# Kernel optimization log

Hardware: AMD Instinct MI355X
Metric: run time of the kernel (lower is better)

Reference implementation:

```python
import jax, jax.numpy as jnp
import numpy as np

N, E, D, G = 20000, 640000, 256, 64
BN_EPS = 1e-5


def setup_inputs() -> dict:
    key = jax.random.key(0)
    ks = jax.random.split(key, 16)
    p = lambda k, sh: jax.random.normal(k, sh, dtype=jnp.float32) * 0.05
    x = jax.random.normal(ks[0], (N, D), dtype=jnp.float32)
    edge_index = jax.random.randint(ks[1], (2, E), 0, N, dtype=jnp.int32)
    batch = jnp.sort(jax.random.randint(ks[2], (N,), 0, G, dtype=jnp.int32))
    return dict(
        x=x, edge_index=edge_index, batch=batch,
        W1=p(ks[3], (D, D)), a1_src=p(ks[4], (D,)), a1_dst=p(ks[5], (D,)), b1=p(ks[6], (D,)),
        W2=p(ks[7], (D, D)), a2_src=p(ks[8], (D,)), a2_dst=p(ks[9], (D,)), b2=p(ks[10], (D,)),
        bn_gamma=jnp.ones((D,), jnp.float32), bn_beta=jnp.zeros((D,), jnp.float32),
        bn_mean=jnp.zeros((D,), jnp.float32), bn_var=jnp.ones((D,), jnp.float32),
        Wl=p(ks[11], (D, D)), bl=p(ks[12], (D,)),
    )


def gat_conv(x, src, dst, W, a_src, a_dst, b):
    # PyG GATConv, heads=1, concat=True, negative_slope=0.2, self-loops already appended
    h = x @ W                               # [N, D]
    alpha_s = h @ a_src                     # [N]
    alpha_d = h @ a_dst                     # [N]
    e = jax.nn.leaky_relu(alpha_s[src] + alpha_d[dst], 0.2)   # [E+N]
    # segment softmax over edges grouped by destination node
    m = jax.ops.segment_max(e, dst, num_segments=N)
    ex = jnp.exp(e - m[dst])
    s = jax.ops.segment_sum(ex, dst, num_segments=N)
    alpha = ex / s[dst]                     # self-loops guarantee s > 0
    out = jax.ops.segment_sum(alpha[:, None] * h[src], dst, num_segments=N)
    return out + b


def reference(x, edge_index, batch, W1, a1_src, a1_dst, b1, W2, a2_src, a2_dst, b2,
              bn_gamma, bn_beta, bn_mean, bn_var, Wl, bl):
    loop = jnp.arange(N, dtype=edge_index.dtype)
    src = jnp.concatenate([edge_index[0], loop])
    dst = jnp.concatenate([edge_index[1], loop])

    h = jax.nn.leaky_relu(gat_conv(x, src, dst, W1, a1_src, a1_dst, b1), 0.01)
    h = jax.nn.leaky_relu(gat_conv(h, src, dst, W2, a2_src, a2_dst, b2), 0.01)
    # BatchNorm over nodes (eval mode, running stats)
    h = (h - bn_mean) * jax.lax.rsqrt(bn_var + BN_EPS) * bn_gamma + bn_beta
    # global mean pool per graph, then linear (dropout is identity in eval)
    sums = jax.ops.segment_sum(h, batch, num_segments=G)           # [G, D]
    cnt = jax.ops.segment_sum(jnp.ones((N,), h.dtype), batch, num_segments=G)
    pooled = sums / jnp.maximum(cnt, 1.0)[:, None]
    return pooled @ Wl.T + bl
```

## Files before the change

### kernel.cpp

```cpp
#include <hip/hip_runtime.h>
#include <hip/hip_bf16.h>

#define NN 20000
#define EE 640000
#define DD 256
#define GG 64
#define ETOT (EE + NN)
#define BN_EPS 1e-5f

#define NPART 8
#define PBLK  128
#define CE    (EE / PBLK)
#define PRNG  (NN / NPART)

#define GBM 64
#define GBN 128
#define GBK 64
#define NGEMMB 626

typedef short s16x8 __attribute__((ext_vector_type(8)));
typedef float f32x4 __attribute__((ext_vector_type(4)));
typedef int   i32x2 __attribute__((ext_vector_type(2)));

__device__ __forceinline__ unsigned short f2bf_hi(float x) {
    unsigned u = __float_as_uint(x);
    unsigned r = (u + 0x7FFFu + ((u >> 16) & 1u)) >> 16;
    return (unsigned short)r;
}
__device__ __forceinline__ float bf2f(unsigned short h) {
    return __uint_as_float(((unsigned)h) << 16);
}

__device__ __forceinline__ void gemm_body(short* As_h, short* As_l,
                                          short* Bs_h, short* Bs_l,
                                          int gx, int gy,
                                          const float* __restrict__ A,
                                          const short* __restrict__ BhT,
                                          const short* __restrict__ BlT,
                                          const float* __restrict__ a_src,
                                          const float* __restrict__ a_dst,
                                          short* __restrict__ hb,
                                          float* __restrict__ asp,
                                          float* __restrict__ adp, int M) {
    int tid = threadIdx.x;
    int row0 = gy * GBM;
    int col0 = gx * GBN;
    int w = tid >> 6, lane = tid & 63;
    int wr = w >> 1, wc = w & 1;

    f32x4 acc[2][4];
    #pragma unroll
    for (int m = 0; m < 2; ++m)
        #pragma unroll
        for (int n = 0; n < 4; ++n)
            acc[m][n] = (f32x4){0.f, 0.f, 0.f, 0.f};

    int srow = tid >> 3;
    int sslot = tid & 7;

    for (int k0 = 0; k0 < DD; k0 += GBK) {
        __syncthreads();
        #pragma unroll
        for (int p = 0; p < 2; ++p) {
            int r = p * 32 + srow;
            int gr = row0 + r;
            float xv[8];
            if (gr < M) {
                const float4* ap = (const float4*)(A + (size_t)gr * DD + k0 + sslot * 8);
                float4 a0 = ap[0], a1 = ap[1];
                xv[0] = a0.x; xv[1] = a0.y; xv[2] = a0.z; xv[3] = a0.w;
                xv[4] = a1.x; xv[5] = a1.y; xv[6] = a1.z; xv[7] = a1.w;
            } else {
                #pragma unroll
                for (int i = 0; i < 8; ++i) xv[i] = 0.f;
            }
            s16x8 hv, lv;
            #pragma unroll
            for (int i = 0; i < 8; ++i) {
                unsigned short hbb = f2bf_hi(xv[i]);
                hv[i] = (short)hbb;
                lv[i] = (short)f2bf_hi(xv[i] - bf2f(hbb));
            }
            int byte = r * 128 + ((sslot ^ (r & 7)) << 4);
            *(s16x8*)((char*)As_h + byte) = hv;
            *(s16x8*)((char*)As_l + byte) = lv;
        }
        #pragma unroll
        for (int p = 0; p < 4; ++p) {
            int r = p * 32 + srow;
            int byte = r * 128 + ((sslot ^ (r & 7)) << 4);
            const short* bhp = BhT + (size_t)(col0 + r) * DD + k0 + sslot * 8;
            const short* blp = BlT + (size_t)(col0 + r) * DD + k0 + sslot * 8;
            *(s16x8*)((char*)Bs_h + byte) = *(const s16x8*)bhp;
            *(s16x8*)((char*)Bs_l + byte) = *(const s16x8*)blp;
        }
        __syncthreads();

        #pragma unroll
        for (int ks = 0; ks < 2; ++ks) {
            s16x8 ah[2], al[2], bh[4], bl[4];
            int g = ks * 4 + (lane >> 4);
            #pragma unroll
            for (int m = 0; m < 2; ++m) {
                int r = wr * 32 + m * 16 + (lane & 15);
                int byte = r * 128 + ((g ^ (r & 7)) << 4);
                ah[m] = *(const s16x8*)((char*)As_h + byte);
                al[m] = *(const s16x8*)((char*)As_l + byte);
            }
            #pragma unroll
            for (int n = 0; n < 4; ++n) {
                int c = wc * 64 + n * 16 + (lane & 15);
                int byte = c * 128 + ((g ^ (c & 7)) << 4);
                bh[n] = *(const s16x8*)((char*)Bs_h + byte);
                bl[n] = *(const s16x8*)((char*)Bs_l + byte);
            }
            #pragma unroll
            for (int m = 0; m < 2; ++m)
                #pragma unroll
                for (int n = 0; n < 4; ++n) {
                    acc[m][n] = __builtin_amdgcn_mfma_f32_16x16x32_bf16(ah[m], bh[n], acc[m][n], 0, 0, 0);
                    acc[m][n] = __builtin_amdgcn_mfma_f32_16x16x32_bf16(ah[m], bl[n], acc[m][n], 0, 0, 0);
                    acc[m][n] = __builtin_amdgcn_mfma_f32_16x16x32_bf16(al[m], bh[n], acc[m][n], 0, 0, 0);
                }
        }
    }

    float vsrc[4], vdst[4];
    #pragma unroll
    for (int n = 0; n < 4; ++n) {
        int cg = col0 + wc * 64 + n * 16 + (lane & 15);
        vsrc[n] = a_src[cg];
        vdst[n] = a_dst[cg];
    }
    #pragma unroll
    for (int m = 0; m < 2; ++m) {
        #pragma unroll
        for (int j = 0; j < 4; ++j) {
            float ps = 0.f, pd = 0.f;
            #pragma unroll
            for (int n = 0; n < 4; ++n) {
                float c = acc[m][n][j];
                ps += c * vsrc[n];
                pd += c * vdst[n];
            }
            #pragma unroll
            for (int o = 1; o < 16; o <<= 1) {
                ps += __shfl_xor(ps, o, 64);
                pd += __shfl_xor(pd, o, 64);
            }
            if ((lane & 15) == 0) {
                int rg = row0 + wr * 32 + m * 16 + ((lane >> 4) << 2) + j;
                if (rg < M) {
                    asp[(size_t)(gx * 2 + wc) * NN + rg] = ps;
                    adp[(size_t)(gx * 2 + wc) * NN + rg] = pd;
                }
            }
        }
    }

    #pragma unroll
    for (int m = 0; m < 2; ++m) {
        int rbase = row0 + wr * 32 + m * 16 + ((lane >> 4) << 2);
        #pragma unroll
        for (int n = 0; n < 4; ++n) {
            int cg = col0 + wc * 64 + n * 16 + (lane & 15);
            #pragma unroll
            for (int j = 0; j < 4; ++j) {
                int rg = rbase + j;
                if (rg < M) hb[(size_t)rg * DD + cg] = (short)f2bf_hi(acc[m][n][j]);
            }
        }
    }
}

__global__ __launch_bounds__(256) void prep_hist_conv_kernel(
        const int* __restrict__ batch, int* __restrict__ start, float* __restrict__ cntf,
        const int* __restrict__ ei, int* __restrict__ counts,
        const float* __restrict__ W1, const float* __restrict__ W2,
        short* __restrict__ BhT1, short* __restrict__ BlT1,
        short* __restrict__ BhT2, short* __restrict__ BlT2) {
    int b = blockIdx.x;
    int r = b & 15, G = b >> 4;
    if (r < 8) {
        int lo = (b & 7) * PRNG;
        int e0 = G * CE;
        for (int i = e0 + threadIdx.x; i < e0 + CE; i += 256) {
            int d = ei[EE + i];
            if ((unsigned)(d - lo) < (unsigned)PRNG) atomicAdd(&counts[d], 1);
        }
        return;
    }
    int idx = G * 8 + (r - 8);
    if (idx < 512) {
        int n = idx & 255, which = idx >> 8;
        int k = threadIdx.x;
        const float* B = which ? W2 : W1;
        short* Bh = which ? BhT2 : BhT1;
        short* Bl = which ? BlT2 : BlT1;
        float x = B[k * DD + n];
        unsigned short hbv = f2bf_hi(x);
        Bh[n * DD + k] = (short)hbv;
        Bl[n * DD + k] = (short)f2bf_hi(x - bf2f(hbv));
    } else if (idx == 512) {
        int g = threadIdx.x;
        if (g <= GG) {
            if (g == GG) start[GG] = NN;
            else {
                int lo = 0, hi = NN;
                while (lo < hi) { int mid = (lo + hi) >> 1; if (batch[mid] < g) lo = mid + 1; else hi = mid; }
                start[g] = lo;
            }
        }
        __syncthreads();
        if (g < GG) cntf[g] = (float)(start[g + 1] - start[g]);
    }
}

#define SCHUNK 20
__global__ __launch_bounds__(1024) void scan_kernel(const int* __restrict__ counts,
                                                    int* __restrict__ offsets,
                                                    int* __restrict__ cursor) {
    __shared__ int wsums[16];
    int t = threadIdx.x, lane = t & 63, wid = t >> 6;
    int base = t * SCHUNK;
    int loc[SCHUNK];
    int sum = 0;
    #pragma unroll
    for (int i = 0; i < SCHUNK; ++i) {
        int idx = base + i;
        int v = (idx < NN) ? (counts[idx] + 1) : 0;
        loc[i] = sum; sum += v;
    }
    int x = sum;
    #pragma unroll
    for (int o = 1; o < 64; o <<= 1) { int tv = __shfl_up(x, o, 64); if (lane >= o) x += tv; }
    if (lane == 63) wsums[wid] = x;
    __syncthreads();
    if (wid == 0) {
        int wv = (lane < 16) ? wsums[lane] : 0;
        #pragma unroll
        for (int o = 1; o < 16; o <<= 1) { int tv = __shfl_up(wv, o, 64); if (lane >= o) wv += tv; }
        if (lane < 16) wsums[lane] = wv;
    }
    __syncthreads();
    int tbase = (wid ? wsums[wid - 1] : 0) + x - sum;
    #pragma unroll
    for (int i = 0; i < SCHUNK; ++i) {
        int idx = base + i;
        if (idx < NN) { int e = tbase + loc[i]; offsets[idx] = e; cursor[idx] = e; }
    }
    if (t == 0) offsets[NN] = wsums[15];
}

__global__ __launch_bounds__(256) void gemm_scatter_kernel(
        const int* __restrict__ ei, int* __restrict__ cursor, int* __restrict__ csr_src,
        const float* __restrict__ A,
        const short* __restrict__ BhT, const short* __restrict__ BlT,
        const float* __restrict__ a_src, const float* __restrict__ a_dst,
        short* __restrict__ hb, float* __restrict__ asp, float* __restrict__ adp, int M) {
    __shared__ short As_h[GBM * GBK];
    __shared__ short As_l[GBM * GBK];
    __shared__ short Bs_h[GBN * GBK];
    __shared__ short Bs_l[GBN * GBK];
    int b = blockIdx.x;
    int r = b & 15, G = b >> 4;
    if (r < 8) {
        int lo = (b & 7) * PRNG;
        int e0 = G * CE;
        for (int i = e0 + threadIdx.x; i < e0 + CE; i += 256) {
            int d = ei[EE + i];
            if ((unsigned)(d - lo) < (unsigned)PRNG) {
                int pos = atomicAdd(&cursor[d], 1);
                csr_src[pos] = ei[i];
            }
        }
        return;
    }
    int gidx = G * 8 + (r - 8);
    if (gidx >= NGEMMB) return;
    gemm_body(As_h, As_l, Bs_h, Bs_l, gidx & 1, gidx >> 1,
              A, BhT, BlT, a_src, a_dst, hb, asp, adp, M);
}

__global__ __launch_bounds__(256) void gemm_kernel(
        const float* __restrict__ A,
        const short* __restrict__ BhT, const short* __restrict__ BlT,
        const float* __restrict__ a_src, const float* __restrict__ a_dst,
        short* __restrict__ hb, float* __restrict__ asp, float* __restrict__ adp, int M) {
    __shared__ short As_h[GBM * GBK];
    __shared__ short As_l[GBM * GBK];
    __shared__ short Bs_h[GBN * GBK];
    __shared__ short Bs_l[GBN * GBK];
    int gidx = blockIdx.x;
    gemm_body(As_h, As_l, Bs_h, Bs_l, gidx & 1, gidx >> 1,
              A, BhT, BlT, a_src, a_dst, hb, asp, adp, M);
}

__global__ void reduce_kernel(const float* __restrict__ asp, const float* __restrict__ adp,
                              const int* __restrict__ offsets,
                              float* __restrict__ as_, float* __restrict__ ad_,
                              int* __restrict__ csr_src) {
    int i = blockIdx.x * blockDim.x + threadIdx.x;
    if (i < NN) {
        as_[i] = asp[i] + asp[NN + i] + asp[2 * NN + i] + asp[3 * NN + i];
        ad_[i] = adp[i] + adp[NN + i] + adp[2 * NN + i] + adp[3 * NN + i];
        csr_src[offsets[i + 1] - 1] = i;
    }
}

__global__ __launch_bounds__(256) void alpha_kernel(const int* __restrict__ csr_src,
                                                    const int* __restrict__ offsets,
                                                    const float* __restrict__ as_,
                                                    const float* __restrict__ ad_,
                                                    int2* __restrict__ pairs) {
    int tid = threadIdx.x;
    int w = tid >> 6, lane = tid & 63;
    int node = blockIdx.x * 4 + w;
    int off = offsets[node];
    int deg = offsets[node + 1] - off;
    float adn = ad_[node];

    if (deg <= 64) {
        int si = 0; float e = -INFINITY;
        if (lane < deg) {
            si = csr_src[off + lane];
            float t = as_[si] + adn;
            e = (t > 0.f) ? t : 0.2f * t;
        }
        float m = e;
        #pragma unroll
        for (int o = 32; o > 0; o >>= 1) m = fmaxf(m, __shfl_xor(m, o, 64));
        float ex = (lane < deg) ? expf(e - m) : 0.f;
        float s = ex;
        #pragma unroll
        for (int o = 32; o > 0; o >>= 1) s += __shfl_xor(s, o, 64);
        if (lane < deg) {
            int2 p; p.x = si; p.y = __float_as_int(ex / s);
            pairs[off + lane] = p;
        }
        return;
    }

    float m = -INFINITY, s = 0.f;
    for (int cs = 0; cs < deg; cs += 64) {
        int cl = min(64, deg - cs);
        float e = -INFINITY;
        if (lane < cl) {
            int si = csr_src[off + cs + lane];
            float t = as_[si] + adn;
            e = (t > 0.f) ? t : 0.2f * t;
        }
        float cm = e;
        #pragma unroll
        for (int o = 32; o > 0; o >>= 1) cm = fmaxf(cm, __shfl_xor(cm, o, 64));
        float newm = fmaxf(m, cm);
        float ex = (lane < cl) ? expf(e - newm) : 0.f;
        float csum = ex;
        #pragma unroll
        for (int o = 32; o > 0; o >>= 1) csum += __shfl_xor(csum, o, 64);
        s = s * expf(m - newm) + csum;
        m = newm;
    }
    float inv = 1.f / s;
    for (int cs = 0; cs < deg; cs += 64) {
        int cl = min(64, deg - cs);
        if (lane < cl) {
            int si = csr_src[off + cs + lane];
            float t = as_[si] + adn;
            float e = (t > 0.f) ? t : 0.2f * t;
            int2 p; p.x = si; p.y = __float_as_int(expf(e - m) * inv);
            pairs[off + cs + lane] = p;
        }
    }
}

__global__ __launch_bounds__(256) void aggregate_kernel(const short* __restrict__ hb,
                                                        const int2* __restrict__ pairs,
                                                        const int* __restrict__ offsets,
                                                        const float* __restrict__ bias,
                                                        float* __restrict__ out) {
    int tid = threadIdx.x;
    int w = tid >> 6, lane = tid & 63;
    int b = blockIdx.x;
    int sl = b & 3;
    int node = ((b >> 2) << 2) + w;
    int eg = lane >> 3;
    int fl = lane & 7;
    int f0 = sl * 64 + fl * 8;
    int off = offsets[node];
    int deg = offsets[node + 1] - off;
    const i32x2* pp = (const i32x2*)pairs + off;

    float acc[4][8];
    #pragma unroll
    for (int c = 0; c < 4; ++c)
        #pragma unroll
        for (int k = 0; k < 8; ++k) acc[c][k] = 0.f;

    for (int j0 = 0; j0 < deg; j0 += 32) {
        i32x2 q[4];
        float a[4];
        #pragma unroll
        for (int c = 0; c < 4; ++c) {
            int idx = j0 + c * 8 + eg;
            int idxc = (idx < deg) ? idx : 0;
            q[c] = pp[idxc];
            a[c] = (idx < deg) ? __int_as_float(q[c].y) : 0.f;
        }
        #pragma unroll
        for (int c = 0; c < 4; ++c) {
            s16x8 hv = *(const s16x8*)(hb + (size_t)q[c].x * DD + f0);
            #pragma unroll
            for (int k = 0; k < 8; ++k)
                acc[c][k] += a[c] * bf2f((unsigned short)hv[k]);
        }
    }

    f32x4 r0, r1;
    #pragma unroll
    for (int k = 0; k < 8; ++k) {
        float v = (acc[0][k] + acc[1][k]) + (acc[2][k] + acc[3][k]);
        v += __shfl_xor(v, 8, 64);
        v += __shfl_xor(v, 16, 64);
        v += __shfl_xor(v, 32, 64);
        if (k < 4) r0[k] = v; else r1[k - 4] = v;
    }
    if (eg == 0) {
        const f32x4 b0 = *(const f32x4*)(bias + f0);
        const f32x4 b1 = *(const f32x4*)(bias + f0 + 4);
        #pragma unroll
        for (int k = 0; k < 4; ++k) {
            float v0 = r0[k] + b0[k];
            float v1 = r1[k] + b1[k];
            r0[k] = (v0 > 0.f) ? v0 : 0.01f * v0;
            r1[k] = (v1 > 0.f) ? v1 : 0.01f * v1;
        }
        __builtin_nontemporal_store(r0, (f32x4*)(out + (size_t)node * DD + f0));
        __builtin_nontemporal_store(r1, (f32x4*)(out + (size_t)node * DD + f0 + 4));
    }
}

#define PSLICE 8
__global__ __launch_bounds__(256) void pool_kernel(const float* __restrict__ h,
                                                   const int* __restrict__ start,
                                                   float* __restrict__ pool) {
    int g = blockIdx.x >> 3, sl = blockIdx.x & (PSLICE - 1);
    int f = threadIdx.x;
    int s0 = start[g], s1 = start[g + 1];
    float acc = 0.f;
    for (int nd = s0 + sl; nd < s1; nd += PSLICE)
        acc += h[(size_t)nd * DD + f];
    if (acc != 0.f || sl == 0) atomicAdd(&pool[g * DD + f], acc);
}

__global__ __launch_bounds__(256) void final_kernel(const float* __restrict__ pool,
                                                    const float* __restrict__ cnt,
                                                    const float* __restrict__ gam,
                                                    const float* __restrict__ bet,
                                                    const float* __restrict__ mean,
                                                    const float* __restrict__ var,
                                                    const float* __restrict__ Wl,
                                                    const float* __restrict__ bl,
                                                    float* __restrict__ out) {
    __shared__ float p_sh[DD];
    int g = blockIdx.x, j = threadIdx.x;
    float cn = cnt[g];
    float scale = gam[j] * rsqrtf(var[j] + BN_EPS);
    p_sh[j] = (cn > 0.f) ? (pool[g * DD + j] / cn - mean[j]) * scale + bet[j] : 0.f;
    __syncthreads();
    float acc = 0.f;
    for (int fi = 0; fi < DD; ++fi)
        acc += p_sh[fi] * Wl[j * DD + fi];
    out[g * DD + j] = acc + bl[j];
}

extern "C" void kernel_launch(void* const* d_in, const int* in_sizes, int n_in,
                              void* d_out, int out_size, void* d_ws, size_t ws_size,
                              hipStream_t stream) {
    const float* x       = (const float*)d_in[0];
    const int*   ei      = (const int*)d_in[1];
    const int*   batch   = (const int*)d_in[2];
    const float* W1      = (const float*)d_in[3];
    const float* a1_src  = (const float*)d_in[4];
    const float* a1_dst  = (const float*)d_in[5];
    const float* b1      = (const float*)d_in[6];
    const float* W2      = (const float*)d_in[7];
    const float* a2_src  = (const float*)d_in[8];
    const float* a2_dst  = (const float*)d_in[9];
    const float* b2      = (const float*)d_in[10];
    const float* bn_g    = (const float*)d_in[11];
    const float* bn_b    = (const float*)d_in[12];
    const float* bn_m    = (const float*)d_in[13];
    const float* bn_v    = (const float*)d_in[14];
    const float* Wl      = (const float*)d_in[15];
    const float* bl      = (const float*)d_in[16];
    float* out = (float*)d_out;

    char* ws = (char*)d_ws;
    size_t o = 0;
    auto take = [&](size_t bytes) { char* p = ws + o; o += (bytes + 255) & ~(size_t)255; return p; };
    int*   counts  = (int*)  take(NN * 4);
    int*   offsets = (int*)  take((NN + 1) * 4);
    int*   cursor  = (int*)  take(NN * 4);
    int*   csr_src = (int*)  take((size_t)ETOT * 4);
    int2*  pairs   = (int2*) take((size_t)ETOT * 8);
    float* asp     = (float*)take((size_t)4 * NN * 4);
    float* adp     = (float*)take((size_t)4 * NN * 4);
    float* as_     = (float*)take(NN * 4);
    float* ad_     = (float*)take(NN * 4);
    short* hb      = (short*)take((size_t)NN * DD * 2);
    float* bufB    = (float*)take((size_t)NN * DD * 4);
    float* pool    = (float*)take(GG * DD * 4);
    float* cnt     = (float*)take(GG * 4);
    int*   start   = (int*)  take((GG + 1) * 4);
    short* BhT1    = (short*)take((size_t)DD * DD * 2);
    short* BlT1    = (short*)take((size_t)DD * DD * 2);
    short* BhT2    = (short*)take((size_t)DD * DD * 2);
    short* BlT2    = (short*)take((size_t)DD * DD * 2);
    (void)ws_size; (void)in_sizes; (void)n_in; (void)out_size;

    hipMemsetAsync(counts, 0, NN * 4, stream);
    hipMemsetAsync(pool, 0, GG * DD * 4, stream);

    prep_hist_conv_kernel<<<2048, 256, 0, stream>>>(batch, start, cnt, ei, counts,
                                                    W1, W2, BhT1, BlT1, BhT2, BlT2);
    scan_kernel<<<1, 1024, 0, stream>>>(counts, offsets, cursor);

    gemm_scatter_kernel<<<2048, 256, 0, stream>>>(ei, cursor, csr_src,
                                                  x, BhT1, BlT1, a1_src, a1_dst,
                                                  hb, asp, adp, NN);
    reduce_kernel<<<(NN + 255) / 256, 256, 0, stream>>>(asp, adp, offsets, as_, ad_, csr_src);
    alpha_kernel<<<NN / 4, 256, 0, stream>>>(csr_src, offsets, as_, ad_, pairs);
    aggregate_kernel<<<NN, 256, 0, stream>>>(hb, pairs, offsets, b1, bufB);

    gemm_kernel<<<NGEMMB, 256, 0, stream>>>(bufB, BhT2, BlT2, a2_src, a2_dst, hb, asp, adp, NN);
    reduce_kernel<<<(NN + 255) / 256, 256, 0, stream>>>(asp, adp, offsets, as_, ad_, csr_src);
    alpha_kernel<<<NN / 4, 256, 0, stream>>>(csr_src, offsets, as_, ad_, pairs);
    aggregate_kernel<<<NN, 256, 0, stream>>>(hb, pairs, offsets, b2, bufB);

    pool_kernel<<<GG * PSLICE, 256, 0, stream>>>(bufB, start, pool);
    final_kernel<<<GG, 256, 0, stream>>>(pool, cnt, bn_g, bn_b, bn_m, bn_v, Wl, bl, out);
}
```

Before: 315.5 us.

## Fuse CSR scatter tail into GEMM blocks and software-pipeline aggregate gather

Layer 1's GEMM no longer interleaves with dedicated scatter blocks that each scan edges for a destination partition. Every GEMM block now does its tile and then scatters a contiguous slice of about 1023 edges into the CSR with atomics, so the partition filtering and repeated edge reads go away. The aggregate kernel now uses two accumulators and prefetches the next pair indices one step ahead, with a lighter bf16 unpack. The trade-offs are less memory-level parallelism per step in the gather and atomics to arbitrary destinations across the whole node range.

```diff
diff --git a/kernel.cpp b/kernel.cpp
--- a/kernel.cpp
+++ b/kernel.cpp
@@ -17,10 +17,12 @@
 #define GBN 128
 #define GBK 64
 #define NGEMMB 626
+#define SCE 1023
 
 typedef short s16x8 __attribute__((ext_vector_type(8)));
 typedef float f32x4 __attribute__((ext_vector_type(4)));
 typedef int   i32x2 __attribute__((ext_vector_type(2)));
+typedef int   i32x4 __attribute__((ext_vector_type(4)));
 
 __device__ __forceinline__ unsigned short f2bf_hi(float x) {
     unsigned u = __float_as_uint(x);
@@ -31,145 +33,14 @@
     return __uint_as_float(((unsigned)h) << 16);
 }
 
-__device__ __forceinline__ void gemm_body(short* As_h, short* As_l,
-                                          short* Bs_h, short* Bs_l,
-                                          int gx, int gy,
-                                          const float* __restrict__ A,
-                                          const short* __restrict__ BhT,
-                                          const short* __restrict__ BlT,
-                                          const float* __restrict__ a_src,
-                                          const float* __restrict__ a_dst,
-                                          short* __restrict__ hb,
-                                          float* __restrict__ asp,
-                                          float* __restrict__ adp, int M) {
-    int tid = threadIdx.x;
-    int row0 = gy * GBM;
-    int col0 = gx * GBN;
-    int w = tid >> 6, lane = tid & 63;
-    int wr = w >> 1, wc = w & 1;
-
-    f32x4 acc[2][4];
-    #pragma unroll
-    for (int m = 0; m < 2; ++m)
-        #pragma unroll
-        for (int n = 0; n < 4; ++n)
-            acc[m][n] = (f32x4){0.f, 0.f, 0.f, 0.f};
-
-    int srow = tid >> 3;
-    int sslot = tid & 7;
-
-    for (int k0 = 0; k0 < DD; k0 += GBK) {
-        __syncthreads();
-        #pragma unroll
-        for (int p = 0; p < 2; ++p) {
-            int r = p * 32 + srow;
-            int gr = row0 + r;
-            float xv[8];
-            if (gr < M) {
-                const float4* ap = (const float4*)(A + (size_t)gr * DD + k0 + sslot * 8);
-                float4 a0 = ap[0], a1 = ap[1];
-                xv[0] = a0.x; xv[1] = a0.y; xv[2] = a0.z; xv[3] = a0.w;
-                xv[4] = a1.x; xv[5] = a1.y; xv[6] = a1.z; xv[7] = a1.w;
-            } else {
-                #pragma unroll
-                for (int i = 0; i < 8; ++i) xv[i] = 0.f;
-            }
-            s16x8 hv, lv;
-            #pragma unroll
-            for (int i = 0; i < 8; ++i) {
-                unsigned short hbb = f2bf_hi(xv[i]);
-                hv[i] = (short)hbb;
-                lv[i] = (short)f2bf_hi(xv[i] - bf2f(hbb));
-            }
-            int byte = r * 128 + ((sslot ^ (r & 7)) << 4);
-            *(s16x8*)((char*)As_h + byte) = hv;
-            *(s16x8*)((char*)As_l + byte) = lv;
-        }
-        #pragma unroll
-        for (int p = 0; p < 4; ++p) {
-            int r = p * 32 + srow;
-            int byte = r * 128 + ((sslot ^ (r & 7)) << 4);
-            const short* bhp = BhT + (size_t)(col0 + r) * DD + k0 + sslot * 8;
-            const short* blp = BlT + (size_t)(col0 + r) * DD + k0 + sslot * 8;
-            *(s16x8*)((char*)Bs_h + byte) = *(const s16x8*)bhp;
-            *(s16x8*)((char*)Bs_l + byte) = *(const s16x8*)blp;
-        }
-        __syncthreads();
-
-        #pragma unroll
-        for (int ks = 0; ks < 2; ++ks) {
-            s16x8 ah[2], al[2], bh[4], bl[4];
-            int g = ks * 4 + (lane >> 4);
-            #pragma unroll
-            for (int m = 0; m < 2; ++m) {
-                int r = wr * 32 + m * 16 + (lane & 15);
-                int byte = r * 128 + ((g ^ (r & 7)) << 4);
-                ah[m] = *(const s16x8*)((char*)As_h + byte);
-                al[m] = *(const s16x8*)((char*)As_l + byte);
-            }
-            #pragma unroll
-            for (int n = 0; n < 4; ++n) {
-                int c = wc * 64 + n * 16 + (lane & 15);
-                int byte = c * 128 + ((g ^ (c & 7)) << 4);
-                bh[n] = *(const s16x8*)((char*)Bs_h + byte);
-                bl[n] = *(const s16x8*)((char*)Bs_l + byte);
-            }
-            #pragma unroll
-            for (int m = 0; m < 2; ++m)
-                #pragma unroll
-                for (int n = 0; n < 4; ++n) {
-                    acc[m][n] = __builtin_amdgcn_mfma_f32_16x16x32_bf16(ah[m], bh[n], acc[m][n], 0, 0, 0);
-                    acc[m][n] = __builtin_amdgcn_mfma_f32_16x16x32_bf16(ah[m], bl[n], acc[m][n], 0, 0, 0);
-                    acc[m][n] = __builtin_amdgcn_mfma_f32_16x16x32_bf16(al[m], bh[n], acc[m][n], 0, 0, 0);
-                }
-        }
-    }
-
-    float vsrc[4], vdst[4];
-    #pragma unroll
-    for (int n = 0; n < 4; ++n) {
-        int cg = col0 + wc * 64 + n * 16 + (lane & 15);
-        vsrc[n] = a_src[cg];
-        vdst[n] = a_dst[cg];
-    }
-    #pragma unroll
-    for (int m = 0; m < 2; ++m) {
-        #pragma unroll
-        for (int j = 0; j < 4; ++j) {
-            float ps = 0.f, pd = 0.f;
-            #pragma unroll
-            for (int n = 0; n < 4; ++n) {
-                float c = acc[m][n][j];
-                ps += c * vsrc[n];
-                pd += c * vdst[n];
-            }
-            #pragma unroll
-            for (int o = 1; o < 16; o <<= 1) {
-                ps += __shfl_xor(ps, o, 64);
-                pd += __shfl_xor(pd, o, 64);
-            }
-            if ((lane & 15) == 0) {
-                int rg = row0 + wr * 32 + m * 16 + ((lane >> 4) << 2) + j;
-                if (rg < M) {
-                    asp[(size_t)(gx * 2 + wc) * NN + rg] = ps;
-                    adp[(size_t)(gx * 2 + wc) * NN + rg] = pd;
-                }
-            }
-        }
-    }
-
-    #pragma unroll
-    for (int m = 0; m < 2; ++m) {
-        int rbase = row0 + wr * 32 + m * 16 + ((lane >> 4) << 2);
-        #pragma unroll
-        for (int n = 0; n < 4; ++n) {
-            int cg = col0 + wc * 64 + n * 16 + (lane & 15);
-            #pragma unroll
-            for (int j = 0; j < 4; ++j) {
-                int rg = rbase + j;
-                if (rg < M) hb[(size_t)rg * DD + cg] = (short)f2bf_hi(acc[m][n][j]);
-            }
-        }
+__device__ __forceinline__ void fma8(const short* __restrict__ hb, int row, int f0,
+                                     float a, float* acc) {
+    i32x4 hv = *(const i32x4*)(hb + (size_t)row * DD + f0);
+    #pragma unroll
+    for (int k = 0; k < 4; ++k) {
+        unsigned u = (unsigned)hv[k];
+        acc[2 * k]     += a * __uint_as_float(u << 16);
+        acc[2 * k + 1] += a * __uint_as_float(u & 0xFFFF0000u);
     }
 }
 
@@ -252,48 +123,158 @@
     if (t == 0) offsets[NN] = wsums[15];
 }
 
-__global__ __launch_bounds__(256) void gemm_scatter_kernel(
-        const int* __restrict__ ei, int* __restrict__ cursor, int* __restrict__ csr_src,
+template<bool SCAT>
+__global__ __launch_bounds__(256) void gemm_kernel(
         const float* __restrict__ A,
         const short* __restrict__ BhT, const short* __restrict__ BlT,
         const float* __restrict__ a_src, const float* __restrict__ a_dst,
-        short* __restrict__ hb, float* __restrict__ asp, float* __restrict__ adp, int M) {
+        short* __restrict__ hb, float* __restrict__ asp, float* __restrict__ adp, int M,
+        const int* __restrict__ ei, int* __restrict__ cursor, int* __restrict__ csr_src) {
     __shared__ short As_h[GBM * GBK];
     __shared__ short As_l[GBM * GBK];
     __shared__ short Bs_h[GBN * GBK];
     __shared__ short Bs_l[GBN * GBK];
-    int b = blockIdx.x;
-    int r = b & 15, G = b >> 4;
-    if (r < 8) {
-        int lo = (b & 7) * PRNG;
-        int e0 = G * CE;
-        for (int i = e0 + threadIdx.x; i < e0 + CE; i += 256) {
+    int tid = threadIdx.x;
+    int gx = blockIdx.x, gy = blockIdx.y;
+    int row0 = gy * GBM;
+    int col0 = gx * GBN;
+    int w = tid >> 6, lane = tid & 63;
+    int wr = w >> 1, wc = w & 1;
+
+    f32x4 acc[2][4];
+    #pragma unroll
+    for (int m = 0; m < 2; ++m)
+        #pragma unroll
+        for (int n = 0; n < 4; ++n)
+            acc[m][n] = (f32x4){0.f, 0.f, 0.f, 0.f};
+
+    int srow = tid >> 3;
+    int sslot = tid & 7;
+
+    for (int k0 = 0; k0 < DD; k0 += GBK) {
+        __syncthreads();
+        #pragma unroll
+        for (int p = 0; p < 2; ++p) {
+            int r = p * 32 + srow;
+            int gr = row0 + r;
+            float xv[8];
+            if (gr < M) {
+                const float4* ap = (const float4*)(A + (size_t)gr * DD + k0 + sslot * 8);
+                float4 a0 = ap[0], a1 = ap[1];
+                xv[0] = a0.x; xv[1] = a0.y; xv[2] = a0.z; xv[3] = a0.w;
+                xv[4] = a1.x; xv[5] = a1.y; xv[6] = a1.z; xv[7] = a1.w;
+            } else {
+                #pragma unroll
+                for (int i = 0; i < 8; ++i) xv[i] = 0.f;
+            }
+            s16x8 hv, lv;
+            #pragma unroll
+            for (int i = 0; i < 8; ++i) {
+                unsigned short hbb = f2bf_hi(xv[i]);
+                hv[i] = (short)hbb;
+                lv[i] = (short)f2bf_hi(xv[i] - bf2f(hbb));
+            }
+            int byte = r * 128 + ((sslot ^ (r & 7)) << 4);
+            *(s16x8*)((char*)As_h + byte) = hv;
+            *(s16x8*)((char*)As_l + byte) = lv;
+        }
+        #pragma unroll
+        for (int p = 0; p < 4; ++p) {
+            int r = p * 32 + srow;
+            int byte = r * 128 + ((sslot ^ (r & 7)) << 4);
+            const short* bhp = BhT + (size_t)(col0 + r) * DD + k0 + sslot * 8;
+            const short* blp = BlT + (size_t)(col0 + r) * DD + k0 + sslot * 8;
+            *(s16x8*)((char*)Bs_h + byte) = *(const s16x8*)bhp;
+            *(s16x8*)((char*)Bs_l + byte) = *(const s16x8*)blp;
+        }
+        __syncthreads();
+
+        #pragma unroll
+        for (int ks = 0; ks < 2; ++ks) {
+            s16x8 ah[2], al[2], bh[4], bl[4];
+            int g = ks * 4 + (lane >> 4);
+            #pragma unroll
+            for (int m = 0; m < 2; ++m) {
+                int r = wr * 32 + m * 16 + (lane & 15);
+                int byte = r * 128 + ((g ^ (r & 7)) << 4);
+                ah[m] = *(const s16x8*)((char*)As_h + byte);
+                al[m] = *(const s16x8*)((char*)As_l + byte);
+            }
+            #pragma unroll
+            for (int n = 0; n < 4; ++n) {
+                int c = wc * 64 + n * 16 + (lane & 15);
+                int byte = c * 128 + ((g ^ (c & 7)) << 4);
+                bh[n] = *(const s16x8*)((char*)Bs_h + byte);
+                bl[n] = *(const s16x8*)((char*)Bs_l + byte);
+            }
+            #pragma unroll
+            for (int m = 0; m < 2; ++m)
+                #pragma unroll
+                for (int n = 0; n < 4; ++n) {
+                    acc[m][n] = __builtin_amdgcn_mfma_f32_16x16x32_bf16(ah[m], bh[n], acc[m][n], 0, 0, 0);
+                    acc[m][n] = __builtin_amdgcn_mfma_f32_16x16x32_bf16(ah[m], bl[n], acc[m][n], 0, 0, 0);
+                    acc[m][n] = __builtin_amdgcn_mfma_f32_16x16x32_bf16(al[m], bh[n], acc[m][n], 0, 0, 0);
+                }
+        }
+    }
+
+    float vsrc[4], vdst[4];
+    #pragma unroll
+    for (int n = 0; n < 4; ++n) {
+        int cg = col0 + wc * 64 + n * 16 + (lane & 15);
+        vsrc[n] = a_src[cg];
+        vdst[n] = a_dst[cg];
+    }
+    #pragma unroll
+    for (int m = 0; m < 2; ++m) {
+        #pragma unroll
+        for (int j = 0; j < 4; ++j) {
+            float ps = 0.f, pd = 0.f;
+            #pragma unroll
+            for (int n = 0; n < 4; ++n) {
+                float c = acc[m][n][j];
+                ps += c * vsrc[n];
+                pd += c * vdst[n];
+            }
+            #pragma unroll
+            for (int o = 1; o < 16; o <<= 1) {
+                ps += __shfl_xor(ps, o, 64);
+                pd += __shfl_xor(pd, o, 64);
+            }
+            if ((lane & 15) == 0) {
+                int rg = row0 + wr * 32 + m * 16 + ((lane >> 4) << 2) + j;
+                if (rg < M) {
+                    asp[(size_t)(gx * 2 + wc) * NN + rg] = ps;
+                    adp[(size_t)(gx * 2 + wc) * NN + rg] = pd;
+                }
+            }
+        }
+    }
+
+    #pragma unroll
+    for (int m = 0; m < 2; ++m) {
+        int rbase = row0 + wr * 32 + m * 16 + ((lane >> 4) << 2);
+        #pragma unroll
+        for (int n = 0; n < 4; ++n) {
+            int cg = col0 + wc * 64 + n * 16 + (lane & 15);
+            #pragma unroll
+            for (int j = 0; j < 4; ++j) {
+                int rg = rbase + j;
+                if (rg < M) hb[(size_t)rg * DD + cg] = (short)f2bf_hi(acc[m][n][j]);
+            }
+        }
+    }
+
+    if (SCAT) {
+        int bid = gy * 2 + gx;
+        int e0 = bid * SCE;
+        int e1 = min(e0 + SCE, EE);
+        for (int i = e0 + tid; i < e1; i += 256) {
             int d = ei[EE + i];
-            if ((unsigned)(d - lo) < (unsigned)PRNG) {
-                int pos = atomicAdd(&cursor[d], 1);
-                csr_src[pos] = ei[i];
-            }
-        }
-        return;
-    }
-    int gidx = G * 8 + (r - 8);
-    if (gidx >= NGEMMB) return;
-    gemm_body(As_h, As_l, Bs_h, Bs_l, gidx & 1, gidx >> 1,
-              A, BhT, BlT, a_src, a_dst, hb, asp, adp, M);
-}
-
-__global__ __launch_bounds__(256) void gemm_kernel(
-        const float* __restrict__ A,
-        const short* __restrict__ BhT, const short* __restrict__ BlT,
-        const float* __restrict__ a_src, const float* __restrict__ a_dst,
-        short* __restrict__ hb, float* __restrict__ asp, float* __restrict__ adp, int M) {
-    __shared__ short As_h[GBM * GBK];
-    __shared__ short As_l[GBM * GBK];
-    __shared__ short Bs_h[GBN * GBK];
-    __shared__ short Bs_l[GBN * GBK];
-    int gidx = blockIdx.x;
-    gemm_body(As_h, As_l, Bs_h, Bs_l, gidx & 1, gidx >> 1,
-              A, BhT, BlT, a_src, a_dst, hb, asp, adp, M);
+            int pos = atomicAdd(&cursor[d], 1);
+            csr_src[pos] = ei[i];
+        }
+    }
 }
 
 __global__ void reduce_kernel(const float* __restrict__ asp, const float* __restrict__ adp,
@@ -391,35 +372,40 @@
     int deg = offsets[node + 1] - off;
     const i32x2* pp = (const i32x2*)pairs + off;
 
-    float acc[4][8];
-    #pragma unroll
-    for (int c = 0; c < 4; ++c)
-        #pragma unroll
-        for (int k = 0; k < 8; ++k) acc[c][k] = 0.f;
-
-    for (int j0 = 0; j0 < deg; j0 += 32) {
-        i32x2 q[4];
-        float a[4];
-        #pragma unroll
-        for (int c = 0; c < 4; ++c) {
-            int idx = j0 + c * 8 + eg;
-            int idxc = (idx < deg) ? idx : 0;
-            q[c] = pp[idxc];
-            a[c] = (idx < deg) ? __int_as_float(q[c].y) : 0.f;
-        }
-        #pragma unroll
-        for (int c = 0; c < 4; ++c) {
-            s16x8 hv = *(const s16x8*)(hb + (size_t)q[c].x * DD + f0);
-            #pragma unroll
-            for (int k = 0; k < 8; ++k)
-                acc[c][k] += a[c] * bf2f((unsigned short)hv[k]);
+    float accA[8], accB[8];
+    #pragma unroll
+    for (int k = 0; k < 8; ++k) { accA[k] = 0.f; accB[k] = 0.f; }
+
+    int j = 0;
+    i32x2 qA, qB;
+    if (deg >= 16) { qA = pp[eg]; qB = pp[8 + eg]; }
+    for (; j + 32 <= deg; j += 16) {
+        i32x2 nA = pp[j + 16 + eg];
+        i32x2 nB = pp[j + 24 + eg];
+        fma8(hb, qA.x, f0, __int_as_float(qA.y), accA);
+        fma8(hb, qB.x, f0, __int_as_float(qB.y), accB);
+        qA = nA; qB = nB;
+    }
+    if (j + 16 <= deg) {
+        fma8(hb, qA.x, f0, __int_as_float(qA.y), accA);
+        fma8(hb, qB.x, f0, __int_as_float(qB.y), accB);
+        j += 16;
+    }
+    {
+        if (j + eg < deg) {
+            i32x2 p = pp[j + eg];
+            fma8(hb, p.x, f0, __int_as_float(p.y), accA);
+        }
+        if (j + 8 + eg < deg) {
+            i32x2 p = pp[j + 8 + eg];
+            fma8(hb, p.x, f0, __int_as_float(p.y), accB);
         }
     }
 
     f32x4 r0, r1;
     #pragma unroll
     for (int k = 0; k < 8; ++k) {
-        float v = (acc[0][k] + acc[1][k]) + (acc[2][k] + acc[3][k]);
+        float v = accA[k] + accB[k];
         v += __shfl_xor(v, 8, 64);
         v += __shfl_xor(v, 16, 64);
         v += __shfl_xor(v, 32, 64);
@@ -526,14 +512,16 @@
                                                     W1, W2, BhT1, BlT1, BhT2, BlT2);
     scan_kernel<<<1, 1024, 0, stream>>>(counts, offsets, cursor);
 
-    gemm_scatter_kernel<<<2048, 256, 0, stream>>>(ei, cursor, csr_src,
-                                                  x, BhT1, BlT1, a1_src, a1_dst,
-                                                  hb, asp, adp, NN);
+    dim3 ggrid(DD / GBN, (NN + GBM - 1) / GBM);
+
+    gemm_kernel<true><<<ggrid, 256, 0, stream>>>(x, BhT1, BlT1, a1_src, a1_dst,
+                                                 hb, asp, adp, NN, ei, cursor, csr_src);
     reduce_kernel<<<(NN + 255) / 256, 256, 0, stream>>>(asp, adp, offsets, as_, ad_, csr_src);
     alpha_kernel<<<NN / 4, 256, 0, stream>>>(csr_src, offsets, as_, ad_, pairs);
     aggregate_kernel<<<NN, 256, 0, stream>>>(hb, pairs, offsets, b1, bufB);
 
-    gemm_kernel<<<NGEMMB, 256, 0, stream>>>(bufB, BhT2, BlT2, a2_src, a2_dst, hb, asp, adp, NN);
+    gemm_kernel<false><<<ggrid, 256, 0, stream>>>(bufB, BhT2, BlT2, a2_src, a2_dst,
+                                                  hb, asp, adp, NN, nullptr, nullptr, nullptr);
     reduce_kernel<<<(NN + 255) / 256, 256, 0, stream>>>(asp, adp, offsets, as_, ad_, csr_src);
     alpha_kernel<<<NN / 4, 256, 0, stream>>>(csr_src, offsets, as_, ad_, pairs);
     aggregate_kernel<<<NN, 256, 0, stream>>>(hb, pairs, offsets, b2, bufB);
```

Result: faster. 275.0 us (-12.8%).
